# Kernel optimization log

Measured on AMD Instinct MI355X. Metric: run time of the kernel, lower is better.

## Reference

```python
import jax, jax.numpy as jnp
import numpy as np

H = 256          # hidden_dim
D = 64           # dim_dynamic
R = 49           # pooler_resolution ** 2
N = 2000         # bs * num_proposals
EPS = 1e-5


def _ln(x, g, b):
    m = jnp.mean(x, axis=-1, keepdims=True)
    v = jnp.mean(jnp.square(x - m), axis=-1, keepdims=True)
    return (x - m) * jax.lax.rsqrt(v + EPS) * g + b


def setup_inputs() -> dict:
    key = jax.random.key(0)
    ks = jax.random.split(key, 6)
    pro_features = jax.random.normal(ks[0], (1, N, H), dtype=jnp.float32)
    roi_features = jax.random.normal(ks[1], (R, N, H), dtype=jnp.float32)
    # dynamic_layer: Linear(H, num_dynamic * H * D) with num_dynamic = 2
    W_dyn = jax.random.normal(ks[2], (H, 2 * H * D), dtype=jnp.float32) * 0.02
    b_dyn = jnp.zeros((2 * H * D,), dtype=jnp.float32)
    # out_layer: Linear(H * R, H)
    W_out = jax.random.normal(ks[3], (H * R, H), dtype=jnp.float32) * 0.02
    b_out = jnp.zeros((H,), dtype=jnp.float32)
    g1 = jnp.ones((D,), dtype=jnp.float32); b1 = jnp.zeros((D,), dtype=jnp.float32)
    g2 = jnp.ones((H,), dtype=jnp.float32); b2 = jnp.zeros((H,), dtype=jnp.float32)
    g3 = jnp.ones((H,), dtype=jnp.float32); b3 = jnp.zeros((H,), dtype=jnp.float32)
    return {"pro_features": pro_features, "roi_features": roi_features,
            "W_dyn": W_dyn, "b_dyn": b_dyn, "W_out": W_out, "b_out": b_out,
            "g1": g1, "b1": b1, "g2": g2, "b2": b2, "g3": g3, "b3": b3}


def reference(pro_features, roi_features, W_dyn, b_dyn, W_out, b_out,
              g1, b1, g2, b2, g3, b3):
    # roi_features: (R, N, H) -> features: (N, R, H)
    feats = jnp.transpose(roi_features, (1, 0, 2))
    # per-instance dynamic parameters: (N, 2*H*D)
    params = pro_features[0] @ W_dyn + b_dyn
    num_params = H * D
    p1 = params[:, :num_params].reshape(-1, H, D)   # (N, H, D)
    p2 = params[:, num_params:].reshape(-1, D, H)   # (N, D, H)
    f = jnp.einsum('nrh,nhd->nrd', feats, p1)       # bmm 1
    f = jax.nn.relu(_ln(f, g1, b1))
    f = jnp.einsum('nrd,ndh->nrh', f, p2)           # bmm 2
    f = jax.nn.relu(_ln(f, g2, b2))
    f = f.reshape(f.shape[0], R * H)                # flatten(1)
    f = jax.nn.relu(_ln(f @ W_out + b_out, g3, b3))
    return f  # (N, H)
```

## Files before the change

### kernel.cpp

```cpp
#include <hip/hip_runtime.h>

typedef unsigned short u16;
typedef __attribute__((ext_vector_type(8))) short short8;
typedef __attribute__((ext_vector_type(4))) float f32x4;

#define N_INST 2000
#define H_DIM 256
#define D_DIM 64
#define R_DIM 49
#define LN_EPS 1e-5f
#define SPLITK 14

__device__ __forceinline__ u16 f2bf(float f) {
  union { float f; unsigned int i; } x; x.f = f;
  unsigned int r = x.i + 0x7fffu + ((x.i >> 16) & 1u);
  return (u16)(r >> 16);
}
__device__ __forceinline__ float bf2f(u16 u) {
  union { unsigned int i; float f; } x; x.i = ((unsigned int)u) << 16; return x.f;
}
__device__ __forceinline__ short8 ld8(const u16* p) {
  return *reinterpret_cast<const short8*>(p);
}
__device__ __forceinline__ short8 pack8(float4 a, float4 b) {
  short8 r;
  r[0] = (short)f2bf(a.x); r[1] = (short)f2bf(a.y);
  r[2] = (short)f2bf(a.z); r[3] = (short)f2bf(a.w);
  r[4] = (short)f2bf(b.x); r[5] = (short)f2bf(b.y);
  r[6] = (short)f2bf(b.z); r[7] = (short)f2bf(b.w);
  return r;
}
__device__ __forceinline__ f32x4 mfma16(short8 a, short8 b, f32x4 c) {
  return __builtin_amdgcn_mfma_f32_16x16x32_bf16(a, b, c, 0, 0, 0);
}
__device__ __forceinline__ void wave_reduce2(float& s, float& s2) {
#pragma unroll
  for (int off = 32; off > 0; off >>= 1) {
    s  += __shfl_down(s, off);
    s2 += __shfl_down(s2, off);
  }
  s = __shfl(s, 0); s2 = __shfl(s2, 0);
}
__device__ __forceinline__ void gload16(const u16* g, u16* l) {
  __builtin_amdgcn_global_load_lds(
      (const __attribute__((address_space(1))) void*)g,
      (__attribute__((address_space(3))) void*)l, 16, 0, 0);
}

__global__ __launch_bounds__(256) void cast_pro(const float* __restrict__ in,
                                                u16* __restrict__ out, int n4) {
  for (int i = blockIdx.x * 256 + threadIdx.x; i < n4; i += gridDim.x * 256) {
    float4 v = ((const float4*)in)[i];
    u16* op = out + i * 4;
    op[0] = f2bf(v.x); op[1] = f2bf(v.y); op[2] = f2bf(v.z); op[3] = f2bf(v.w);
  }
}

__global__ __launch_bounds__(256) void cast_wdyn(const float* __restrict__ W,
                                                 u16* __restrict__ WT) {
  __shared__ u16 T[64][65];
  const int tid = threadIdx.x;
  const int wave = tid >> 6, lane = tid & 63;
  const int half = blockIdx.x >> 10;
  const int b = blockIdx.x & 1023;
  const int kt = b >> 8;
  long colbase, rowbase; int rstride;
  if (half == 0) {
    int h = b & 255;
    colbase = (long)h * 64; rowbase = h; rstride = 256;
  } else {
    int d = b & 63, hc = (b >> 6) & 3;
    colbase = 16384L + d * 256 + hc * 64;
    rowbase = 16384L + hc * 4096 + d; rstride = 64;
  }
#pragma unroll
  for (int i = 0; i < 16; ++i) {
    int kk = wave * 16 + i;
    int k = kt * 64 + kk;
    T[kk][lane] = f2bf(W[(long)k * 32768 + colbase + lane]);
  }
  __syncthreads();
#pragma unroll
  for (int i = 0; i < 16; ++i) {
    int jj = wave * 16 + i;
    long ro = rowbase + (long)jj * rstride;
    WT[ro * 256 + kt * 64 + lane] = T[lane][jj];
  }
}

__global__ __launch_bounds__(256) void cast_wout(const float* __restrict__ W,
                                                 u16* __restrict__ WT) {
  __shared__ u16 T[64][65];
  const int tid = threadIdx.x;
  const int wave = tid >> 6, lane = tid & 63;
  const int kt = blockIdx.x >> 2, ct = blockIdx.x & 3;
#pragma unroll
  for (int i = 0; i < 16; ++i) {
    int kk = wave * 16 + i;
    long k = (long)kt * 64 + kk;
    T[kk][lane] = f2bf(W[k * 256 + ct * 64 + lane]);
  }
  __syncthreads();
#pragma unroll
  for (int i = 0; i < 16; ++i) {
    int cc = wave * 16 + i;
    long c = (long)ct * 64 + cc;
    WT[c * 12544 + (long)kt * 64 + lane] = T[lane][cc];
  }
}

__global__ __launch_bounds__(256, 3) void gemm128(
    const u16* __restrict__ A, int lda, int M,
    const u16* __restrict__ BT, int ldbt,
    const float* __restrict__ bias, int bias_mode,
    void* __restrict__ Cout, int ldc, long c_stride_s,
    int ksteps, int n_blocks, int out_f32)
{
  union Smem {
    struct { u16 a[2][128 * 32]; u16 b[2][128 * 32]; } s;
    u16 cb[128 * 128];
  };
  __shared__ Smem sm;

  const int tid = threadIdx.x;
  const int wave = tid >> 6, lane = tid & 63;
  const int quad = lane >> 4, l16 = lane & 15;
  const int wm = wave >> 1, wn = wave & 1;
  const int bid = blockIdx.x;
  const int mblk = bid / n_blocks, nblk = bid - mblk * n_blocks;
  const int m0 = mblk * 128, n0 = nblk * 128;
  const int s = blockIdx.y;
  const int kb = s * ksteps * 32;

  const int cl = tid & 3;
  const int r0 = tid >> 2, r1 = 64 + (tid >> 2);
  const int cg0 = cl ^ ((r0 >> 1) & 3);
  const int cg1 = cl ^ ((r1 >> 1) & 3);
  int ga0 = m0 + r0; if (ga0 >= M) ga0 = M - 1;
  int ga1 = m0 + r1; if (ga1 >= M) ga1 = M - 1;
  const u16* gA0 = A + (long)ga0 * lda + kb + cg0 * 8;
  const u16* gA1 = A + (long)ga1 * lda + kb + cg1 * 8;
  const u16* gB0 = BT + (long)(n0 + r0) * ldbt + kb + cg0 * 8;
  const u16* gB1 = BT + (long)(n0 + r1) * ldbt + kb + cg1 * 8;

  int fAoff[4], fBoff[4];
#pragma unroll
  for (int i = 0; i < 4; ++i) {
    int rt = wm * 64 + i * 16 + l16;
    fAoff[i] = rt * 32 + (quad ^ ((rt >> 1) & 3)) * 8;
    int ct = wn * 64 + i * 16 + l16;
    fBoff[i] = ct * 32 + (quad ^ ((ct >> 1) & 3)) * 8;
  }

  f32x4 acc[4][4];
#pragma unroll
  for (int mi = 0; mi < 4; ++mi)
#pragma unroll
    for (int ni = 0; ni < 4; ++ni) acc[mi][ni] = f32x4{0.f, 0.f, 0.f, 0.f};

  gload16(gA0, &sm.s.a[0][tid * 8]);
  gload16(gA1, &sm.s.a[0][(tid + 256) * 8]);
  gload16(gB0, &sm.s.b[0][tid * 8]);
  gload16(gB1, &sm.s.b[0][(tid + 256) * 8]);

  for (int ks = 0; ks < ksteps; ++ks) {
    const int cur = ks & 1, nxt = cur ^ 1;
    __syncthreads();
    if (ks + 1 < ksteps) {
      const int ko = (ks + 1) * 32;
      gload16(gA0 + ko, &sm.s.a[nxt][tid * 8]);
      gload16(gA1 + ko, &sm.s.a[nxt][(tid + 256) * 8]);
      gload16(gB0 + ko, &sm.s.b[nxt][tid * 8]);
      gload16(gB1 + ko, &sm.s.b[nxt][(tid + 256) * 8]);
    }
    short8 av[4], bv[4];
#pragma unroll
    for (int i = 0; i < 4; ++i) {
      av[i] = ld8(&sm.s.a[cur][fAoff[i]]);
      bv[i] = ld8(&sm.s.b[cur][fBoff[i]]);
    }
#pragma unroll
    for (int mi = 0; mi < 4; ++mi)
#pragma unroll
      for (int ni = 0; ni < 4; ++ni)
        acc[mi][ni] = mfma16(av[mi], bv[ni], acc[mi][ni]);
  }

  if (!out_f32) {
    float bvv[4];
#pragma unroll
    for (int ni = 0; ni < 4; ++ni) {
      int col = n0 + wn * 64 + ni * 16 + l16;
      int bi = col;
      if (bias_mode == 3)
        bi = (col < 16384) ? (((col & 255) << 6) + (col >> 8))
                           : (16384 + ((col & 63) << 8) + ((col >> 6) & 255));
      bvv[ni] = bias ? bias[bi] : 0.f;
    }
    __syncthreads();
#pragma unroll
    for (int mi = 0; mi < 4; ++mi)
#pragma unroll
      for (int ni = 0; ni < 4; ++ni)
#pragma unroll
        for (int i = 0; i < 4; ++i) {
          int row = wm * 64 + mi * 16 + quad * 4 + i;
          int col = wn * 64 + ni * 16 + l16;
          sm.cb[row * 128 + col] = f2bf(acc[mi][ni][i] + bvv[ni]);
        }
    __syncthreads();
    u16* Cp = (u16*)Cout;
#pragma unroll
    for (int j = 0; j < 8; ++j) {
      int lin = j * 2048 + tid * 8;
      int row = lin >> 7, col = lin & 127;
      int grow = m0 + row;
      if (grow < M)
        *reinterpret_cast<short8*>(Cp + (long)grow * ldc + n0 + col) =
            ld8(&sm.cb[lin]);
    }
  } else {
    float* Cp = (float*)Cout + (long)s * c_stride_s;
#pragma unroll
    for (int mi = 0; mi < 4; ++mi)
#pragma unroll
      for (int ni = 0; ni < 4; ++ni) {
        int col = n0 + wn * 64 + ni * 16 + l16;
#pragma unroll
        for (int i = 0; i < 4; ++i) {
          int row = m0 + wm * 64 + mi * 16 + quad * 4 + i;
          if (row < M) Cp[(long)row * ldc + col] = acc[mi][ni][i];
        }
      }
  }
}

__global__ __launch_bounds__(256, 4) void bmm12_ln(
    const float* __restrict__ roi,
    const u16* __restrict__ P12,
    const float* __restrict__ g1, const float* __restrict__ b1,
    const float* __restrict__ g2, const float* __restrict__ b2,
    u16* __restrict__ f2n)
{
  __shared__ __align__(16) u16 p1b[16384];
  __shared__ __align__(16) u16 f1b[4096];
  const int n = blockIdx.x;
  const int tid = threadIdx.x;
  const int wave = tid >> 6, lane = tid & 63;
  const int quad = lane >> 4, l16 = lane & 15;
  const int wstripe = wave * 16;

  const u16* P1n = P12 + (long)n * 32768;
#pragma unroll
  for (int j = 0; j < 8; ++j) {
    int lc = j * 256 + tid;
    int d = lc >> 5, c = lc & 31;
    int cg = (c & 24) | ((c & 7) ^ (d & 7));
    gload16(P1n + d * 256 + cg * 8, &p1b[lc * 8]);
  }
  int r = wstripe + l16;
  int rr = (r < R_DIM) ? r : 0;
  const float* Arow = roi + ((long)rr * N_INST + n) * H_DIM + quad * 8;
  short8 sa[8];
#pragma unroll
  for (int ks = 0; ks < 8; ++ks) {
    float4 va = ((const float4*)(Arow + ks * 32))[0];
    float4 vb = ((const float4*)(Arow + ks * 32))[1];
    sa[ks] = pack8(va, vb);
  }
  const u16* P2n = P12 + (long)n * 32768 + 16384;
  short8 pf[4][2];
#pragma unroll
  for (int hs = 0; hs < 4; ++hs)
#pragma unroll
    for (int ks = 0; ks < 2; ++ks) {
      int h = wave * 64 + hs * 16 + l16;
      pf[hs][ks] = ld8(P2n + h * 64 + (ks * 4 + quad) * 8);
    }
  float gv1[4], bv1[4];
#pragma unroll
  for (int sub = 0; sub < 4; ++sub) {
    gv1[sub] = g1[sub * 16 + l16]; bv1[sub] = b1[sub * 16 + l16];
  }
  __syncthreads();

  f32x4 acc1[4];
#pragma unroll
  for (int i = 0; i < 4; ++i) acc1[i] = f32x4{0.f, 0.f, 0.f, 0.f};
#pragma unroll
  for (int ks = 0; ks < 8; ++ks) {
#pragma unroll
    for (int sub = 0; sub < 4; ++sub) {
      int d = sub * 16 + l16;
      int q = ks * 4 + quad;
      int c = (q & 24) | ((q & 7) ^ (d & 7));
      acc1[sub] = mfma16(sa[ks], ld8(&p1b[d * 256 + c * 8]), acc1[sub]);
    }
  }

  {
    float s1[4], s2[4];
#pragma unroll
    for (int i = 0; i < 4; ++i) {
      s1[i] = 0.f; s2[i] = 0.f;
#pragma unroll
      for (int sub = 0; sub < 4; ++sub) {
        float v = acc1[sub][i]; s1[i] += v; s2[i] += v * v;
      }
    }
#pragma unroll
    for (int m = 1; m < 16; m <<= 1)
#pragma unroll
      for (int i = 0; i < 4; ++i) {
        s1[i] += __shfl_xor(s1[i], m, 16);
        s2[i] += __shfl_xor(s2[i], m, 16);
      }
#pragma unroll
    for (int i = 0; i < 4; ++i) {
      float mean = s1[i] * (1.f / 64.f);
      float var = s2[i] * (1.f / 64.f) - mean * mean;
      float rs = rsqrtf(var + LN_EPS);
      int row = wstripe + quad * 4 + i;
#pragma unroll
      for (int sub = 0; sub < 4; ++sub) {
        float y = fmaxf((acc1[sub][i] - mean) * rs * gv1[sub] + bv1[sub], 0.f);
        int kc = (sub * 2 + (l16 >> 3)) ^ (row & 7);
        f1b[row * 64 + kc * 8 + (l16 & 7)] = f2bf(y);
      }
    }
  }
  __syncthreads();

  f32x4 acc2[4][4];
#pragma unroll
  for (int rs = 0; rs < 4; ++rs)
#pragma unroll
    for (int hs = 0; hs < 4; ++hs) acc2[rs][hs] = f32x4{0.f, 0.f, 0.f, 0.f};
#pragma unroll
  for (int ks = 0; ks < 2; ++ks) {
#pragma unroll
    for (int rs = 0; rs < 4; ++rs) {
      int row = rs * 16 + l16;
      int c2 = (ks * 4 + quad) ^ (row & 7);
      short8 af = ld8(&f1b[row * 64 + c2 * 8]);
#pragma unroll
      for (int hs = 0; hs < 4; ++hs)
        acc2[rs][hs] = mfma16(af, pf[hs][ks], acc2[rs][hs]);
    }
  }

  float s1[4][4], s2[4][4];
#pragma unroll
  for (int rs = 0; rs < 4; ++rs)
#pragma unroll
    for (int i = 0; i < 4; ++i) {
      float a = 0.f, b = 0.f;
#pragma unroll
      for (int hs = 0; hs < 4; ++hs) {
        float v = acc2[rs][hs][i]; a += v; b += v * v;
      }
      s1[rs][i] = a; s2[rs][i] = b;
    }
#pragma unroll
  for (int m = 1; m < 16; m <<= 1)
#pragma unroll
    for (int rs = 0; rs < 4; ++rs)
#pragma unroll
      for (int i = 0; i < 4; ++i) {
        s1[rs][i] += __shfl_xor(s1[rs][i], m, 16);
        s2[rs][i] += __shfl_xor(s2[rs][i], m, 16);
      }
  float2* lnst = reinterpret_cast<float2*>(&p1b[14336]);
  if (l16 == 0) {
#pragma unroll
    for (int rs = 0; rs < 4; ++rs)
#pragma unroll
      for (int i = 0; i < 4; ++i) {
        int row = rs * 16 + quad * 4 + i;
        lnst[row * 4 + wave] = float2{s1[rs][i], s2[rs][i]};
      }
  }
  __syncthreads();

#pragma unroll
  for (int rs = 0; rs < 4; ++rs)
#pragma unroll
    for (int i = 0; i < 4; ++i) {
      int row = rs * 16 + quad * 4 + i;
      f32x4 qa = *reinterpret_cast<const f32x4*>(&lnst[row * 4]);
      f32x4 qb = *reinterpret_cast<const f32x4*>(&lnst[row * 4 + 2]);
      float S1 = qa[0] + qa[2] + qb[0] + qb[2];
      float S2 = qa[1] + qa[3] + qb[1] + qb[3];
      float mean = S1 * (1.f / 256.f);
      float var = S2 * (1.f / 256.f) - mean * mean;
      float rsq = rsqrtf(var + LN_EPS);
      if (row < R_DIM) {
#pragma unroll
        for (int hs = 0; hs < 4; ++hs)
          p1b[row * 264 + wave * 64 + hs * 16 + l16] =
              f2bf((acc2[rs][hs][i] - mean) * rsq);
      }
    }
  __syncthreads();

  u16* f2out = f2n + (long)n * (R_DIM * H_DIM);
  for (int t = tid; t < R_DIM * 32; t += 256) {
    int row = t >> 5, c = t & 31;
    short8 z8 = ld8(&p1b[row * 264 + c * 8]);
    const float4* gp = (const float4*)(g2 + c * 8);
    const float4* bp = (const float4*)(b2 + c * 8);
    float4 ga = gp[0], gb = gp[1], ba = bp[0], bb = bp[1];
    short8 y;
    y[0] = (short)f2bf(fmaxf(bf2f((u16)z8[0]) * ga.x + ba.x, 0.f));
    y[1] = (short)f2bf(fmaxf(bf2f((u16)z8[1]) * ga.y + ba.y, 0.f));
    y[2] = (short)f2bf(fmaxf(bf2f((u16)z8[2]) * ga.z + ba.z, 0.f));
    y[3] = (short)f2bf(fmaxf(bf2f((u16)z8[3]) * ga.w + ba.w, 0.f));
    y[4] = (short)f2bf(fmaxf(bf2f((u16)z8[4]) * gb.x + bb.x, 0.f));
    y[5] = (short)f2bf(fmaxf(bf2f((u16)z8[5]) * gb.y + bb.y, 0.f));
    y[6] = (short)f2bf(fmaxf(bf2f((u16)z8[6]) * gb.z + bb.z, 0.f));
    y[7] = (short)f2bf(fmaxf(bf2f((u16)z8[7]) * gb.w + bb.w, 0.f));
    *reinterpret_cast<short8*>(f2out + row * 256 + c * 8) = y;
  }
}

__global__ __launch_bounds__(64) void ln3_k(
    const float* __restrict__ partial,
    const float* __restrict__ b_out,
    const float* __restrict__ g3, const float* __restrict__ b3,
    float* __restrict__ out)
{
  const int n = blockIdx.x;
  const int lane = threadIdx.x;
  float x[4], sv = 0.f, s2 = 0.f;
#pragma unroll
  for (int j = 0; j < 4; ++j) {
    int h = lane + 64 * j;
    float v = b_out[h];
#pragma unroll
    for (int ss = 0; ss < SPLITK; ++ss)
      v += partial[((long)ss * N_INST + n) * H_DIM + h];
    x[j] = v; sv += v; s2 += v * v;
  }
  wave_reduce2(sv, s2);
  float mean = sv * (1.f / 256.f);
  float var = s2 * (1.f / 256.f) - mean * mean;
  float rs = rsqrtf(var + LN_EPS);
#pragma unroll
  for (int j = 0; j < 4; ++j) {
    int h = lane + 64 * j;
    float y = fmaxf((x[j] - mean) * rs * g3[h] + b3[h], 0.f);
    out[(long)n * H_DIM + h] = y;
  }
}

extern "C" void kernel_launch(void* const* d_in, const int* in_sizes, int n_in,
                              void* d_out, int out_size, void* d_ws, size_t ws_size,
                              hipStream_t stream) {
  const float* pro  = (const float*)d_in[0];
  const float* roi  = (const float*)d_in[1];
  const float* Wdyn = (const float*)d_in[2];
  const float* bdyn = (const float*)d_in[3];
  const float* Wout = (const float*)d_in[4];
  const float* bout = (const float*)d_in[5];
  const float* g1 = (const float*)d_in[6];
  const float* b1 = (const float*)d_in[7];
  const float* g2 = (const float*)d_in[8];
  const float* b2 = (const float*)d_in[9];
  const float* g3 = (const float*)d_in[10];
  const float* b3 = (const float*)d_in[11];
  float* out = (float*)d_out;

  char* ws = (char*)d_ws;
  u16* proB  = (u16*)ws;
  u16* WdynT = (u16*)(ws + 1024000);
  u16* WoutT = (u16*)(ws + 17801216);
  u16* P12   = (u16*)(ws + 24223744);
  u16* f2n   = (u16*)(ws + 155295744);
  float* partial = (float*)(ws + 24223744);

  dim3 blk(256);

  cast_pro<<<dim3(500), blk, 0, stream>>>(pro, proB, 512000 / 4);
  cast_wdyn<<<dim3(2048), blk, 0, stream>>>(Wdyn, WdynT);
  cast_wout<<<dim3(784), blk, 0, stream>>>(Wout, WoutT);

  gemm128<<<dim3(16 * 256, 1), blk, 0, stream>>>(
      proB, H_DIM, N_INST, WdynT, H_DIM, bdyn, 3,
      (void*)P12, 32768, 0L, 8, 256, 0);
  bmm12_ln<<<dim3(N_INST), blk, 0, stream>>>(roi, P12, g1, b1, g2, b2, f2n);
  gemm128<<<dim3(16 * 2, SPLITK), blk, 0, stream>>>(
      f2n, R_DIM * H_DIM, N_INST, WoutT, R_DIM * H_DIM, nullptr, 0,
      (void*)partial, H_DIM, (long)N_INST * H_DIM, 28, 2, 1);
  ln3_k<<<dim3(N_INST), dim3(64), 0, stream>>>(partial, bout, g3, b3, out);
}
```

Before: 326.4 us.

## Merge prep casts into one kernel and use 256x128 tiles for the param GEMM

The three cast/transpose kernels are merged into one prep_all launch that picks its job by block index. The dynamic-parameter GEMM moves to a dedicated 512-thread kernel with 256x128 tiles, so each B tile loaded from global memory is reused across twice as many rows. The aim is fewer launches and less B-operand traffic for the large 2000x32768 output. The cost is a bigger shared-memory footprint that allows only one block per CU, and wasted padding rows because 2000 is not a multiple of 256.

```diff
diff --git a/kernel.cpp b/kernel.cpp
--- a/kernel.cpp
+++ b/kernel.cpp
@@ -47,79 +47,174 @@
       (__attribute__((address_space(3))) void*)l, 16, 0, 0);
 }
 
-__global__ __launch_bounds__(256) void cast_pro(const float* __restrict__ in,
-                                                u16* __restrict__ out, int n4) {
-  for (int i = blockIdx.x * 256 + threadIdx.x; i < n4; i += gridDim.x * 256) {
-    float4 v = ((const float4*)in)[i];
-    u16* op = out + i * 4;
-    op[0] = f2bf(v.x); op[1] = f2bf(v.y); op[2] = f2bf(v.z); op[3] = f2bf(v.w);
-  }
-}
-
-__global__ __launch_bounds__(256) void cast_wdyn(const float* __restrict__ W,
-                                                 u16* __restrict__ WT) {
+__global__ __launch_bounds__(256) void prep_all(
+    const float* __restrict__ pro,  u16* __restrict__ proB,
+    const float* __restrict__ Wdyn, u16* __restrict__ WdynT,
+    const float* __restrict__ Wout, u16* __restrict__ WoutT) {
   __shared__ u16 T[64][65];
   const int tid = threadIdx.x;
   const int wave = tid >> 6, lane = tid & 63;
-  const int half = blockIdx.x >> 10;
-  const int b = blockIdx.x & 1023;
-  const int kt = b >> 8;
-  long colbase, rowbase; int rstride;
-  if (half == 0) {
-    int h = b & 255;
-    colbase = (long)h * 64; rowbase = h; rstride = 256;
+  const int b = blockIdx.x;
+  if (b < 2048) {
+    const int half = b >> 10;
+    const int bb = b & 1023;
+    const int kt = bb >> 8;
+    long colbase, rowbase; int rstride;
+    if (half == 0) {
+      int h = bb & 255;
+      colbase = (long)h * 64; rowbase = h; rstride = 256;
+    } else {
+      int d = bb & 63, hc = (bb >> 6) & 3;
+      colbase = 16384L + d * 256 + hc * 64;
+      rowbase = 16384L + hc * 4096 + d; rstride = 64;
+    }
+#pragma unroll
+    for (int i = 0; i < 16; ++i) {
+      int kk = wave * 16 + i;
+      int k = kt * 64 + kk;
+      T[kk][lane] = f2bf(Wdyn[(long)k * 32768 + colbase + lane]);
+    }
+    __syncthreads();
+#pragma unroll
+    for (int i = 0; i < 16; ++i) {
+      int jj = wave * 16 + i;
+      long ro = rowbase + (long)jj * rstride;
+      WdynT[ro * 256 + kt * 64 + lane] = T[lane][jj];
+    }
+  } else if (b < 2832) {
+    const int b2 = b - 2048;
+    const int kt = b2 >> 2, ct = b2 & 3;
+#pragma unroll
+    for (int i = 0; i < 16; ++i) {
+      int kk = wave * 16 + i;
+      long k = (long)kt * 64 + kk;
+      T[kk][lane] = f2bf(Wout[k * 256 + ct * 64 + lane]);
+    }
+    __syncthreads();
+#pragma unroll
+    for (int i = 0; i < 16; ++i) {
+      int cc = wave * 16 + i;
+      long c = (long)ct * 64 + cc;
+      WoutT[c * 12544 + (long)kt * 64 + lane] = T[lane][cc];
+    }
   } else {
-    int d = b & 63, hc = (b >> 6) & 3;
-    colbase = 16384L + d * 256 + hc * 64;
-    rowbase = 16384L + hc * 4096 + d; rstride = 64;
-  }
-#pragma unroll
-  for (int i = 0; i < 16; ++i) {
-    int kk = wave * 16 + i;
-    int k = kt * 64 + kk;
-    T[kk][lane] = f2bf(W[(long)k * 32768 + colbase + lane]);
-  }
-  __syncthreads();
-#pragma unroll
-  for (int i = 0; i < 16; ++i) {
-    int jj = wave * 16 + i;
-    long ro = rowbase + (long)jj * rstride;
-    WT[ro * 256 + kt * 64 + lane] = T[lane][jj];
-  }
-}
-
-__global__ __launch_bounds__(256) void cast_wout(const float* __restrict__ W,
-                                                 u16* __restrict__ WT) {
-  __shared__ u16 T[64][65];
+    const int n4 = 128000;
+    for (int i = (b - 2832) * 256 + tid; i < n4; i += 500 * 256) {
+      float4 v = ((const float4*)pro)[i];
+      u16* op = proB + i * 4;
+      op[0] = f2bf(v.x); op[1] = f2bf(v.y); op[2] = f2bf(v.z); op[3] = f2bf(v.w);
+    }
+  }
+}
+
+__global__ __launch_bounds__(512, 1) void gemm256p(
+    const u16* __restrict__ A,
+    const u16* __restrict__ BT,
+    const float* __restrict__ bias,
+    u16* __restrict__ C)
+{
+  union Smem {
+    struct { u16 a[2][256 * 32]; u16 b[2][128 * 32]; } s;
+    u16 cb[256 * 128];
+  };
+  __shared__ Smem sm;
+
   const int tid = threadIdx.x;
   const int wave = tid >> 6, lane = tid & 63;
-  const int kt = blockIdx.x >> 2, ct = blockIdx.x & 3;
-#pragma unroll
-  for (int i = 0; i < 16; ++i) {
-    int kk = wave * 16 + i;
-    long k = (long)kt * 64 + kk;
-    T[kk][lane] = f2bf(W[k * 256 + ct * 64 + lane]);
+  const int quad = lane >> 4, l16 = lane & 15;
+  const int wm = wave >> 1, wn = wave & 1;
+  const int bid = blockIdx.x;
+  const int mblk = bid >> 8, nblk = bid & 255;
+  const int m0 = mblk * 256, n0 = nblk * 128;
+
+  const int ca = tid & 3;
+  const int ra = tid >> 2;
+  const int cg = ca ^ ((ra >> 1) & 3);
+  int gr0 = m0 + ra;       if (gr0 >= N_INST) gr0 = N_INST - 1;
+  int gr1 = m0 + 128 + ra; if (gr1 >= N_INST) gr1 = N_INST - 1;
+  const u16* gA0 = A + (long)gr0 * 256 + cg * 8;
+  const u16* gA1 = A + (long)gr1 * 256 + cg * 8;
+  const u16* gB0 = BT + (long)(n0 + ra) * 256 + cg * 8;
+
+  int fAoff[4], fBoff[4];
+#pragma unroll
+  for (int i = 0; i < 4; ++i) {
+    int rt = wm * 64 + i * 16 + l16;
+    fAoff[i] = rt * 32 + (quad ^ ((rt >> 1) & 3)) * 8;
+    int ct = wn * 64 + i * 16 + l16;
+    fBoff[i] = ct * 32 + (quad ^ ((ct >> 1) & 3)) * 8;
+  }
+
+  f32x4 acc[4][4];
+#pragma unroll
+  for (int mi = 0; mi < 4; ++mi)
+#pragma unroll
+    for (int ni = 0; ni < 4; ++ni) acc[mi][ni] = f32x4{0.f, 0.f, 0.f, 0.f};
+
+  gload16(gA0, &sm.s.a[0][tid * 8]);
+  gload16(gA1, &sm.s.a[0][(tid + 512) * 8]);
+  gload16(gB0, &sm.s.b[0][tid * 8]);
+
+  for (int ks = 0; ks < 8; ++ks) {
+    const int cur = ks & 1, nxt = cur ^ 1;
+    __syncthreads();
+    if (ks + 1 < 8) {
+      const int ko = (ks + 1) * 32;
+      gload16(gA0 + ko, &sm.s.a[nxt][tid * 8]);
+      gload16(gA1 + ko, &sm.s.a[nxt][(tid + 512) * 8]);
+      gload16(gB0 + ko, &sm.s.b[nxt][tid * 8]);
+    }
+    short8 av[4], bv[4];
+#pragma unroll
+    for (int i = 0; i < 4; ++i) {
+      av[i] = ld8(&sm.s.a[cur][fAoff[i]]);
+      bv[i] = ld8(&sm.s.b[cur][fBoff[i]]);
+    }
+#pragma unroll
+    for (int mi = 0; mi < 4; ++mi)
+#pragma unroll
+      for (int ni = 0; ni < 4; ++ni)
+        acc[mi][ni] = mfma16(av[mi], bv[ni], acc[mi][ni]);
+  }
+
+  float bvv[4];
+#pragma unroll
+  for (int ni = 0; ni < 4; ++ni) {
+    int col = n0 + wn * 64 + ni * 16 + l16;
+    int bi = (col < 16384) ? (((col & 255) << 6) + (col >> 8))
+                           : (16384 + ((col & 63) << 8) + ((col >> 6) & 255));
+    bvv[ni] = bias[bi];
   }
   __syncthreads();
 #pragma unroll
-  for (int i = 0; i < 16; ++i) {
-    int cc = wave * 16 + i;
-    long c = (long)ct * 64 + cc;
-    WT[c * 12544 + (long)kt * 64 + lane] = T[lane][cc];
+  for (int mi = 0; mi < 4; ++mi)
+#pragma unroll
+    for (int ni = 0; ni < 4; ++ni)
+#pragma unroll
+      for (int i = 0; i < 4; ++i) {
+        int row = wm * 64 + mi * 16 + quad * 4 + i;
+        int col = wn * 64 + ni * 16 + l16;
+        sm.cb[row * 128 + col] = f2bf(acc[mi][ni][i] + bvv[ni]);
+      }
+  __syncthreads();
+#pragma unroll
+  for (int j = 0; j < 8; ++j) {
+    int lin = j * 4096 + tid * 8;
+    int row = lin >> 7, col = lin & 127;
+    int grow = m0 + row;
+    if (grow < N_INST)
+      *reinterpret_cast<short8*>(C + (long)grow * 32768 + n0 + col) =
+          ld8(&sm.cb[lin]);
   }
 }
 
 __global__ __launch_bounds__(256, 3) void gemm128(
     const u16* __restrict__ A, int lda, int M,
     const u16* __restrict__ BT, int ldbt,
-    const float* __restrict__ bias, int bias_mode,
     void* __restrict__ Cout, int ldc, long c_stride_s,
-    int ksteps, int n_blocks, int out_f32)
+    int ksteps, int n_blocks)
 {
-  union Smem {
-    struct { u16 a[2][128 * 32]; u16 b[2][128 * 32]; } s;
-    u16 cb[128 * 128];
-  };
+  struct Smem { u16 a[2][128 * 32]; u16 b[2][128 * 32]; };
   __shared__ Smem sm;
 
   const int tid = threadIdx.x;
@@ -158,26 +253,26 @@
 #pragma unroll
     for (int ni = 0; ni < 4; ++ni) acc[mi][ni] = f32x4{0.f, 0.f, 0.f, 0.f};
 
-  gload16(gA0, &sm.s.a[0][tid * 8]);
-  gload16(gA1, &sm.s.a[0][(tid + 256) * 8]);
-  gload16(gB0, &sm.s.b[0][tid * 8]);
-  gload16(gB1, &sm.s.b[0][(tid + 256) * 8]);
+  gload16(gA0, &sm.a[0][tid * 8]);
+  gload16(gA1, &sm.a[0][(tid + 256) * 8]);
+  gload16(gB0, &sm.b[0][tid * 8]);
+  gload16(gB1, &sm.b[0][(tid + 256) * 8]);
 
   for (int ks = 0; ks < ksteps; ++ks) {
     const int cur = ks & 1, nxt = cur ^ 1;
     __syncthreads();
     if (ks + 1 < ksteps) {
       const int ko = (ks + 1) * 32;
-      gload16(gA0 + ko, &sm.s.a[nxt][tid * 8]);
-      gload16(gA1 + ko, &sm.s.a[nxt][(tid + 256) * 8]);
-      gload16(gB0 + ko, &sm.s.b[nxt][tid * 8]);
-      gload16(gB1 + ko, &sm.s.b[nxt][(tid + 256) * 8]);
+      gload16(gA0 + ko, &sm.a[nxt][tid * 8]);
+      gload16(gA1 + ko, &sm.a[nxt][(tid + 256) * 8]);
+      gload16(gB0 + ko, &sm.b[nxt][tid * 8]);
+      gload16(gB1 + ko, &sm.b[nxt][(tid + 256) * 8]);
     }
     short8 av[4], bv[4];
 #pragma unroll
     for (int i = 0; i < 4; ++i) {
-      av[i] = ld8(&sm.s.a[cur][fAoff[i]]);
-      bv[i] = ld8(&sm.s.b[cur][fBoff[i]]);
+      av[i] = ld8(&sm.a[cur][fAoff[i]]);
+      bv[i] = ld8(&sm.b[cur][fBoff[i]]);
     }
 #pragma unroll
     for (int mi = 0; mi < 4; ++mi)
@@ -186,53 +281,18 @@
         acc[mi][ni] = mfma16(av[mi], bv[ni], acc[mi][ni]);
   }
 
-  if (!out_f32) {
-    float bvv[4];
+  float* Cp = (float*)Cout + (long)s * c_stride_s;
+#pragma unroll
+  for (int mi = 0; mi < 4; ++mi)
 #pragma unroll
     for (int ni = 0; ni < 4; ++ni) {
       int col = n0 + wn * 64 + ni * 16 + l16;
-      int bi = col;
-      if (bias_mode == 3)
-        bi = (col < 16384) ? (((col & 255) << 6) + (col >> 8))
-                           : (16384 + ((col & 63) << 8) + ((col >> 6) & 255));
-      bvv[ni] = bias ? bias[bi] : 0.f;
-    }
-    __syncthreads();
-#pragma unroll
-    for (int mi = 0; mi < 4; ++mi)
-#pragma unroll
-      for (int ni = 0; ni < 4; ++ni)
-#pragma unroll
-        for (int i = 0; i < 4; ++i) {
-          int row = wm * 64 + mi * 16 + quad * 4 + i;
-          int col = wn * 64 + ni * 16 + l16;
-          sm.cb[row * 128 + col] = f2bf(acc[mi][ni][i] + bvv[ni]);
-        }
-    __syncthreads();
-    u16* Cp = (u16*)Cout;
-#pragma unroll
-    for (int j = 0; j < 8; ++j) {
-      int lin = j * 2048 + tid * 8;
-      int row = lin >> 7, col = lin & 127;
-      int grow = m0 + row;
-      if (grow < M)
-        *reinterpret_cast<short8*>(Cp + (long)grow * ldc + n0 + col) =
-            ld8(&sm.cb[lin]);
-    }
-  } else {
-    float* Cp = (float*)Cout + (long)s * c_stride_s;
-#pragma unroll
-    for (int mi = 0; mi < 4; ++mi)
-#pragma unroll
-      for (int ni = 0; ni < 4; ++ni) {
-        int col = n0 + wn * 64 + ni * 16 + l16;
-#pragma unroll
-        for (int i = 0; i < 4; ++i) {
-          int row = m0 + wm * 64 + mi * 16 + quad * 4 + i;
-          if (row < M) Cp[(long)row * ldc + col] = acc[mi][ni][i];
-        }
-      }
-  }
+#pragma unroll
+      for (int i = 0; i < 4; ++i) {
+        int row = m0 + wm * 64 + mi * 16 + quad * 4 + i;
+        if (row < M) Cp[(long)row * ldc + col] = acc[mi][ni][i];
+      }
+    }
 }
 
 __global__ __launch_bounds__(256, 4) void bmm12_ln(
@@ -480,16 +540,15 @@
 
   dim3 blk(256);
 
-  cast_pro<<<dim3(500), blk, 0, stream>>>(pro, proB, 512000 / 4);
-  cast_wdyn<<<dim3(2048), blk, 0, stream>>>(Wdyn, WdynT);
-  cast_wout<<<dim3(784), blk, 0, stream>>>(Wout, WoutT);
-
-  gemm128<<<dim3(16 * 256, 1), blk, 0, stream>>>(
-      proB, H_DIM, N_INST, WdynT, H_DIM, bdyn, 3,
-      (void*)P12, 32768, 0L, 8, 256, 0);
+  prep_all<<<dim3(3332), blk, 0, stream>>>(pro, proB, Wdyn, WdynT, Wout, WoutT);
+
+  gemm256p<<<dim3(2048), dim3(512), 0, stream>>>(proB, WdynT, bdyn, P12);
+
   bmm12_ln<<<dim3(N_INST), blk, 0, stream>>>(roi, P12, g1, b1, g2, b2, f2n);
+
   gemm128<<<dim3(16 * 2, SPLITK), blk, 0, stream>>>(
-      f2n, R_DIM * H_DIM, N_INST, WoutT, R_DIM * H_DIM, nullptr, 0,
-      (void*)partial, H_DIM, (long)N_INST * H_DIM, 28, 2, 1);
+      f2n, R_DIM * H_DIM, N_INST, WoutT, R_DIM * H_DIM,
+      (void*)partial, H_DIM, (long)N_INST * H_DIM, 28, 2);
+
   ln3_k<<<dim3(N_INST), dim3(64), 0, stream>>>(partial, bout, g3, b3, out);
 }
```

Result: slower. 333.3 us (+2.1%).
